# Performance work log

Measured on AMD Instinct MI355X. Metric: run time of the kernel, lower is better.

The kernel has to match this reference:

```python
import jax, jax.numpy as jnp
import numpy as np

N_NODES = 100000
N_EDGES = 1600000
IN_DIM = 128
OUT_DIM = 64


def setup_inputs() -> dict:
    key = jax.random.key(0)
    k1, k2, k3, k4, k5 = jax.random.split(key, 5)
    X = jax.random.normal(k1, (N_NODES, IN_DIM), dtype=jnp.float32)
    # reset_parameters: uniform(-stdv, stdv), stdv = 1/sqrt(output_dim)
    stdv = 1.0 / np.sqrt(OUT_DIM)
    weights = jax.random.uniform(k2, (IN_DIM, OUT_DIM), dtype=jnp.float32,
                                 minval=-stdv, maxval=stdv)
    attention_w = jax.random.normal(k3, (1, 1), dtype=jnp.float32)
    edge_src = jnp.sort(jax.random.randint(k4, (N_EDGES,), 0, N_NODES, dtype=jnp.int32))
    edge_dst = jax.random.randint(k5, (N_EDGES,), 0, N_NODES, dtype=jnp.int32)
    return {"X": X, "weights": weights, "attention_w": attention_w,
            "edge_src": edge_src, "edge_dst": edge_dst}


def reference(X, weights, attention_w, edge_src, edge_dst):
    # Dense projection: X_prime = X @ W  -> [N, OUT_DIM]
    X_prime = X @ weights
    # forward_ef: per-edge scalar feature = <X_prime[src], X_prime[dst]>  -> [E]
    src_feat = X_prime[edge_src]          # [E, OUT_DIM] irregular gather
    dst_feat = X_prime[edge_dst]          # [E, OUT_DIM] irregular gather
    edge_feature = jnp.einsum('ed,ed->e', src_feat, dst_feat)
    # edge_attentions = edge_feature[:, None] @ attention_w -> [n_heads=1, E]
    att = edge_feature * attention_w[0, 0]            # [E]
    # forward_AGNN: out[i] = sum_{e:(i->j)} att[e] * X_prime[j]
    msgs = att[:, None] * dst_feat                    # [E, OUT_DIM]
    out = jax.ops.segment_sum(msgs, edge_src, num_segments=X.shape[0])
    return out
```

## Files before the change

kernel.cpp:

```cpp
#include <hip/hip_runtime.h>
#include <stdint.h>

#define N_NODES 100000
#define N_EDGES 1600000
#define IN_DIM 128
#define OUT_DIM 64

typedef __bf16    bf16x8 __attribute__((ext_vector_type(8)));
typedef float     f32x4  __attribute__((ext_vector_type(4)));
typedef _Float16  h2     __attribute__((ext_vector_type(2)));

__device__ __forceinline__ uint16_t f2bf(float f) {
    uint32_t u = __float_as_uint(f);
    return (uint16_t)((u + 0x7fffu + ((u >> 16) & 1u)) >> 16);
}
__device__ __forceinline__ float hdot8(uint4 a, uint4 b, float c) {
#if __has_builtin(__builtin_amdgcn_fdot2)
    c = __builtin_amdgcn_fdot2(__builtin_bit_cast(h2, a.x), __builtin_bit_cast(h2, b.x), c, false);
    c = __builtin_amdgcn_fdot2(__builtin_bit_cast(h2, a.y), __builtin_bit_cast(h2, b.y), c, false);
    c = __builtin_amdgcn_fdot2(__builtin_bit_cast(h2, a.z), __builtin_bit_cast(h2, b.z), c, false);
    c = __builtin_amdgcn_fdot2(__builtin_bit_cast(h2, a.w), __builtin_bit_cast(h2, b.w), c, false);
#else
    const h2 qa[4] = {__builtin_bit_cast(h2,a.x),__builtin_bit_cast(h2,a.y),
                      __builtin_bit_cast(h2,a.z),__builtin_bit_cast(h2,a.w)};
    const h2 qb[4] = {__builtin_bit_cast(h2,b.x),__builtin_bit_cast(h2,b.y),
                      __builtin_bit_cast(h2,b.z),__builtin_bit_cast(h2,b.w)};
    #pragma unroll
    for (int i = 0; i < 4; ++i) {
        c = fmaf((float)qa[i][0], (float)qb[i][0], c);
        c = fmaf((float)qa[i][1], (float)qb[i][1], c);
    }
#endif
    return c;
}

__global__ __launch_bounds__(256) void prep(const int* __restrict__ src,
                                            const float* __restrict__ W,
                                            int* __restrict__ row_ptr,
                                            uint4* __restrict__ Wfrag) {
    const int b = blockIdx.x;
    if (b < N_EDGES / 256) {
        int e = b * 256 + threadIdx.x;
        int s = src[e];
        if (e == 0) {
            for (int i = 0; i <= s; ++i) row_ptr[i] = 0;
        } else {
            int sp = src[e - 1];
            for (int i = sp + 1; i <= s; ++i) row_ptr[i] = e;
        }
        if (e == N_EDGES - 1) {
            for (int i = s + 1; i <= N_NODES; ++i) row_ptr[i] = N_EDGES;
        }
    } else {
        int item = (b - N_EDGES / 256) * 256 + threadIdx.x;
        if (item < 1024) {
            int f = item >> 6, lane = item & 63;
            int ct = f >> 2, ks = f & 3;
            int col = ct * 16 + (lane & 15);
            int kb  = ks * 32 + (lane >> 4) * 8;
            uint32_t u[4];
            #pragma unroll
            for (int j = 0; j < 4; ++j) {
                uint32_t lo = f2bf(W[(kb + 2 * j)     * OUT_DIM + col]);
                uint32_t hi = f2bf(W[(kb + 2 * j + 1) * OUT_DIM + col]);
                u[j] = lo | (hi << 16);
            }
            Wfrag[f * 64 + lane] = make_uint4(u[0], u[1], u[2], u[3]);
        }
    }
}

__global__ __launch_bounds__(256) void gemm_xw(const float* __restrict__ X,
                                               const uint4* __restrict__ Wfrag,
                                               _Float16* __restrict__ XPh,
                                               int nRows) {
    const int t = threadIdx.x;
    const int lane = t & 63;

    bf16x8 bfr[16];
    #pragma unroll
    for (int f = 0; f < 16; ++f)
        bfr[f] = __builtin_bit_cast(bf16x8, Wfrag[f * 64 + lane]);

    const int rowBase = blockIdx.x * 64 + (t >> 6) * 16;
    const int r  = rowBase + (lane & 15);
    const int kb = (lane >> 4) * 8;
    const bool inb = r < nRows;

    f32x4 acc[4] = {{0,0,0,0},{0,0,0,0},{0,0,0,0},{0,0,0,0}};

    #pragma unroll
    for (int ks = 0; ks < 4; ++ks) {
        float4 x0 = make_float4(0.f,0.f,0.f,0.f), x1 = x0;
        if (inb) {
            const float* p = &X[(size_t)r * IN_DIM + ks * 32 + kb];
            x0 = *(const float4*)&p[0];
            x1 = *(const float4*)&p[4];
        }
        bf16x8 a;
        a[0]=(__bf16)x0.x; a[1]=(__bf16)x0.y; a[2]=(__bf16)x0.z; a[3]=(__bf16)x0.w;
        a[4]=(__bf16)x1.x; a[5]=(__bf16)x1.y; a[6]=(__bf16)x1.z; a[7]=(__bf16)x1.w;
        #pragma unroll
        for (int ct = 0; ct < 4; ++ct)
            acc[ct] = __builtin_amdgcn_mfma_f32_16x16x32_bf16(a, bfr[ct * 4 + ks], acc[ct], 0, 0, 0);
    }

    const int orow = rowBase + (lane >> 4) * 4;
    const int ocol = lane & 15;
    #pragma unroll
    for (int ct = 0; ct < 4; ++ct) {
        #pragma unroll
        for (int rr = 0; rr < 4; ++rr) {
            int gr = orow + rr;
            if (gr < nRows) XPh[(size_t)gr * OUT_DIM + ct * 16 + ocol] = (_Float16)acc[ct][rr];
        }
    }
}

__global__ __launch_bounds__(256, 8) void agnn_edge(const _Float16* __restrict__ XPh,
                                                    const int* __restrict__ row_ptr,
                                                    const int* __restrict__ dst,
                                                    const float* __restrict__ aw,
                                                    float* __restrict__ out) {
    const int t    = threadIdx.x;
    const int lane = t & 63;
    const int g    = lane >> 3;
    const int sl   = lane & 7;
    const int node = blockIdx.x * 32 + (t >> 6) * 8 + g;

    const int lo = row_ptr[node];
    const int hi = row_ptr[node + 1];

    const uint4 q = *(const uint4*)&XPh[(size_t)node * OUT_DIM + sl * 8];
    float acc[8] = {0.f,0.f,0.f,0.f,0.f,0.f,0.f,0.f};

    int  e   = lo;
    bool act = e < hi;
    int  d   = dst[act ? e : 0];
    uint4 xd = *(const uint4*)&XPh[(size_t)d * OUT_DIM + sl * 8];

    while (true) {
        const int  en   = e + 1;
        const bool actn = en < hi;
        const int  dn   = dst[actn ? en : 0];
        const uint4 xdn = *(const uint4*)&XPh[(size_t)dn * OUT_DIM + sl * 8];

        float p = hdot8(q, xd, 0.f);
        p += __shfl_xor(p, 1);
        p += __shfl_xor(p, 2);
        p += __shfl_xor(p, 4);
        p = act ? p : 0.f;
        const h2 d0 = __builtin_bit_cast(h2, xd.x);
        const h2 d1 = __builtin_bit_cast(h2, xd.y);
        const h2 d2 = __builtin_bit_cast(h2, xd.z);
        const h2 d3 = __builtin_bit_cast(h2, xd.w);
        acc[0] = fmaf(p, (float)d0[0], acc[0]);
        acc[1] = fmaf(p, (float)d0[1], acc[1]);
        acc[2] = fmaf(p, (float)d1[0], acc[2]);
        acc[3] = fmaf(p, (float)d1[1], acc[3]);
        acc[4] = fmaf(p, (float)d2[0], acc[4]);
        acc[5] = fmaf(p, (float)d2[1], acc[5]);
        acc[6] = fmaf(p, (float)d3[0], acc[6]);
        acc[7] = fmaf(p, (float)d3[1], acc[7]);

        e = en; act = actn; xd = xdn;
        if (!__any(act)) break;
    }

    const float a = aw[0];
    float* o = &out[(size_t)node * OUT_DIM + sl * 8];
    *(float4*)&o[0] = make_float4(acc[0]*a, acc[1]*a, acc[2]*a, acc[3]*a);
    *(float4*)&o[4] = make_float4(acc[4]*a, acc[5]*a, acc[6]*a, acc[7]*a);
}

extern "C" void kernel_launch(void* const* d_in, const int* in_sizes, int n_in,
                              void* d_out, int out_size, void* d_ws, size_t ws_size,
                              hipStream_t stream) {
    const float* X   = (const float*)d_in[0];
    const float* W   = (const float*)d_in[1];
    const float* aw  = (const float*)d_in[2];
    const int*   src = (const int*)d_in[3];
    const int*   dst = (const int*)d_in[4];
    float* out = (float*)d_out;

    _Float16* XPh     = (_Float16*)d_ws;
    int*      row_ptr = (int*)((char*)d_ws + (size_t)N_NODES * OUT_DIM * 2);
    uint4*    Wfrag   = (uint4*)((char*)d_ws + 13200016);

    prep<<<N_EDGES / 256 + 4, 256, 0, stream>>>(src, W, row_ptr, Wfrag);
    gemm_xw<<<(N_NODES + 63) / 64, 256, 0, stream>>>(X, Wfrag, XPh, N_NODES);
    agnn_edge<<<N_NODES / 32, 256, 0, stream>>>(XPh, row_ptr, dst, aw, out);
}
```

Before: 69.76 us.

## Quantize projected features to int8 and use sdot4 in the edge kernel

The GEMM kernel now also computes a global max-abs of the projected features through an atomicMax. A new kernel quantizes the fp16 features to int8 with one per-tensor scale. A new edge kernel gathers 8-byte int8 rows instead of 16-byte fp16 rows, computes the edge dot products with sdot4, and prefetches two edges ahead; the output is rescaled by scale^3 times the attention weight. This halves the bytes of the irregular gathers, at the cost of an extra quantize pass, an atomic, and much lower numerical precision from per-tensor int8 quantization.

```diff
diff --git a/kernel.cpp b/kernel.cpp
--- a/kernel.cpp
+++ b/kernel.cpp
@@ -13,6 +13,16 @@
 __device__ __forceinline__ uint16_t f2bf(float f) {
     uint32_t u = __float_as_uint(f);
     return (uint16_t)((u + 0x7fffu + ((u >> 16) & 1u)) >> 16);
+}
+__device__ __forceinline__ int dot4i8(uint32_t a, uint32_t b, int c) {
+#if __has_builtin(__builtin_amdgcn_sdot4)
+    return __builtin_amdgcn_sdot4((int)a, (int)b, c, false);
+#else
+    #pragma unroll
+    for (int k = 0; k < 4; ++k)
+        c += (int)(int8_t)(a >> (8 * k)) * (int)(int8_t)(b >> (8 * k));
+    return c;
+#endif
 }
 __device__ __forceinline__ float hdot8(uint4 a, uint4 b, float c) {
 #if __has_builtin(__builtin_amdgcn_fdot2)
@@ -37,7 +47,8 @@
 __global__ __launch_bounds__(256) void prep(const int* __restrict__ src,
                                             const float* __restrict__ W,
                                             int* __restrict__ row_ptr,
-                                            uint4* __restrict__ Wfrag) {
+                                            uint4* __restrict__ Wfrag,
+                                            unsigned* __restrict__ gmax) {
     const int b = blockIdx.x;
     if (b < N_EDGES / 256) {
         int e = b * 256 + threadIdx.x;
@@ -52,6 +63,7 @@
             for (int i = s + 1; i <= N_NODES; ++i) row_ptr[i] = N_EDGES;
         }
     } else {
+        if (b == N_EDGES / 256 && threadIdx.x == 0) *gmax = 0u;
         int item = (b - N_EDGES / 256) * 256 + threadIdx.x;
         if (item < 1024) {
             int f = item >> 6, lane = item & 63;
@@ -73,6 +85,7 @@
 __global__ __launch_bounds__(256) void gemm_xw(const float* __restrict__ X,
                                                const uint4* __restrict__ Wfrag,
                                                _Float16* __restrict__ XPh,
+                                               unsigned* __restrict__ gmax,
                                                int nRows) {
     const int t = threadIdx.x;
     const int lane = t & 63;
@@ -107,14 +120,105 @@
 
     const int orow = rowBase + (lane >> 4) * 4;
     const int ocol = lane & 15;
+    float m = 0.f;
     #pragma unroll
     for (int ct = 0; ct < 4; ++ct) {
         #pragma unroll
         for (int rr = 0; rr < 4; ++rr) {
             int gr = orow + rr;
             if (gr < nRows) XPh[(size_t)gr * OUT_DIM + ct * 16 + ocol] = (_Float16)acc[ct][rr];
-        }
-    }
+            m = fmaxf(m, fabsf(acc[ct][rr]));
+        }
+    }
+    #pragma unroll
+    for (int off = 1; off < 64; off <<= 1) m = fmaxf(m, __shfl_xor(m, off));
+    if (lane == 0) atomicMax(gmax, __float_as_uint(m));
+}
+
+__global__ __launch_bounds__(256) void quantize(const _Float16* __restrict__ XPh,
+                                                const unsigned* __restrict__ gmax,
+                                                uint2* __restrict__ Q) {
+    const int i = blockIdx.x * 256 + threadIdx.x;
+    const float gm = __uint_as_float(*gmax);
+    const float inv = gm > 0.f ? 127.f / gm : 0.f;
+    uint4 h = ((const uint4*)XPh)[i];
+    uint32_t w[2];
+    #pragma unroll
+    for (int half = 0; half < 2; ++half) {
+        uint32_t res = 0;
+        #pragma unroll
+        for (int j = 0; j < 2; ++j) {
+            uint32_t hw = half == 0 ? (j == 0 ? h.x : h.y) : (j == 0 ? h.z : h.w);
+            h2 p = __builtin_bit_cast(h2, hw);
+            int v0 = (int)rintf((float)p[0] * inv);
+            int v1 = (int)rintf((float)p[1] * inv);
+            res |= ((uint32_t)(uint8_t)(int8_t)v0) << (j * 16);
+            res |= ((uint32_t)(uint8_t)(int8_t)v1) << (j * 16 + 8);
+        }
+        w[half] = res;
+    }
+    Q[i] = make_uint2(w[0], w[1]);
+}
+
+__global__ __launch_bounds__(256, 8) void agnn_edge_q(const uint8_t* __restrict__ Q,
+                                                      const int* __restrict__ row_ptr,
+                                                      const int* __restrict__ dst,
+                                                      const float* __restrict__ aw,
+                                                      const unsigned* __restrict__ gmax,
+                                                      float* __restrict__ out) {
+    const int t    = threadIdx.x;
+    const int lane = t & 63;
+    const int g    = lane >> 3;
+    const int sl   = lane & 7;
+    const int node = blockIdx.x * 32 + (t >> 6) * 8 + g;
+
+    const int lo = row_ptr[node];
+    const int hi = row_ptr[node + 1];
+
+    const uint2 q = *(const uint2*)&Q[(size_t)node * OUT_DIM + sl * 8];
+    float acc[8] = {0.f,0.f,0.f,0.f,0.f,0.f,0.f,0.f};
+
+    int  e1 = lo + 1;
+    bool a0 = lo < hi, a1 = e1 < hi;
+    {
+        int d0 = dst[a0 ? lo : 0];
+        int d1 = dst[a1 ? e1 : 0];
+        uint2 x0 = *(const uint2*)&Q[(size_t)d0 * OUT_DIM + sl * 8];
+        uint2 x1 = *(const uint2*)&Q[(size_t)d1 * OUT_DIM + sl * 8];
+
+        while (__any(a0)) {
+            const int  e2 = e1 + 1;
+            const bool a2 = e2 < hi;
+            const int  d2 = dst[a2 ? e2 : 0];
+            const uint2 x2 = *(const uint2*)&Q[(size_t)d2 * OUT_DIM + sl * 8];
+
+            int p = dot4i8(q.x, x0.x, 0);
+            p     = dot4i8(q.y, x0.y, p);
+            p += __shfl_xor(p, 1);
+            p += __shfl_xor(p, 2);
+            p += __shfl_xor(p, 4);
+            const float pf = a0 ? (float)p : 0.f;
+            const int32_t wx = (int32_t)x0.x, wy = (int32_t)x0.y;
+            acc[0] = fmaf(pf, (float)((wx << 24) >> 24), acc[0]);
+            acc[1] = fmaf(pf, (float)((wx << 16) >> 24), acc[1]);
+            acc[2] = fmaf(pf, (float)((wx <<  8) >> 24), acc[2]);
+            acc[3] = fmaf(pf, (float)( wx        >> 24), acc[3]);
+            acc[4] = fmaf(pf, (float)((wy << 24) >> 24), acc[4]);
+            acc[5] = fmaf(pf, (float)((wy << 16) >> 24), acc[5]);
+            acc[6] = fmaf(pf, (float)((wy <<  8) >> 24), acc[6]);
+            acc[7] = fmaf(pf, (float)( wy        >> 24), acc[7]);
+
+            a0 = a1; x0 = x1;
+            a1 = a2; x1 = x2; e1 = e2;
+        }
+    }
+
+    const float gm = __uint_as_float(*gmax);
+    const float s  = gm * (1.f / 127.f);
+    const float k  = s * s * s * aw[0];
+    float* o = &out[(size_t)node * OUT_DIM + sl * 8];
+    *(float4*)&o[0] = make_float4(acc[0]*k, acc[1]*k, acc[2]*k, acc[3]*k);
+    *(float4*)&o[4] = make_float4(acc[4]*k, acc[5]*k, acc[6]*k, acc[7]*k);
 }
 
 __global__ __launch_bounds__(256, 8) void agnn_edge(const _Float16* __restrict__ XPh,
@@ -184,10 +288,18 @@
     float* out = (float*)d_out;
 
     _Float16* XPh     = (_Float16*)d_ws;
-    int*      row_ptr = (int*)((char*)d_ws + (size_t)N_NODES * OUT_DIM * 2);
+    int*      row_ptr = (int*)((char*)d_ws + 12800000);
     uint4*    Wfrag   = (uint4*)((char*)d_ws + 13200016);
-
-    prep<<<N_EDGES / 256 + 4, 256, 0, stream>>>(src, W, row_ptr, Wfrag);
-    gemm_xw<<<(N_NODES + 63) / 64, 256, 0, stream>>>(X, Wfrag, XPh, N_NODES);
-    agnn_edge<<<N_NODES / 32, 256, 0, stream>>>(XPh, row_ptr, dst, aw, out);
-}
+    unsigned* gmax    = (unsigned*)((char*)d_ws + 13216400);
+    uint8_t*  Q       = (uint8_t*)((char*)d_ws + 13216416);
+
+    prep<<<N_EDGES / 256 + 4, 256, 0, stream>>>(src, W, row_ptr, Wfrag, gmax);
+    gemm_xw<<<(N_NODES + 63) / 64, 256, 0, stream>>>(X, Wfrag, XPh, gmax, N_NODES);
+
+    if (ws_size >= (size_t)19616416) {
+        quantize<<<3125, 256, 0, stream>>>(XPh, gmax, (uint2*)Q);
+        agnn_edge_q<<<N_NODES / 32, 256, 0, stream>>>(Q, row_ptr, dst, aw, gmax, out);
+    } else {
+        agnn_edge<<<N_NODES / 32, 256, 0, stream>>>(XPh, row_ptr, dst, aw, out);
+    }
+}
```

Result: slower. 201.8 us (+189.4%).

## Quantize projected features to int8 with per-row scales and batch edge gathers

Applied to the files above, without the earlier changes.

The projection kernel now stores X_prime as int8 with a per-row absmax scale instead of fp16, halving the bytes per gathered row. The edge kernel loads eight destination indices cooperatively, shuffles them across lanes, issues eight independent gathers per step, and computes dot products with sdot4. This targets gather bandwidth and memory-level parallelism in the irregular edge loop, at the cost of int8 quantization error. The dot product is squared into the output, so that error is amplified and may break accuracy tolerance.

```diff
diff --git a/kernel.cpp b/kernel.cpp
--- a/kernel.cpp
+++ b/kernel.cpp
@@ -8,30 +8,20 @@
 
 typedef __bf16    bf16x8 __attribute__((ext_vector_type(8)));
 typedef float     f32x4  __attribute__((ext_vector_type(4)));
-typedef _Float16  h2     __attribute__((ext_vector_type(2)));
 
 __device__ __forceinline__ uint16_t f2bf(float f) {
     uint32_t u = __float_as_uint(f);
     return (uint16_t)((u + 0x7fffu + ((u >> 16) & 1u)) >> 16);
 }
-__device__ __forceinline__ float hdot8(uint4 a, uint4 b, float c) {
-#if __has_builtin(__builtin_amdgcn_fdot2)
-    c = __builtin_amdgcn_fdot2(__builtin_bit_cast(h2, a.x), __builtin_bit_cast(h2, b.x), c, false);
-    c = __builtin_amdgcn_fdot2(__builtin_bit_cast(h2, a.y), __builtin_bit_cast(h2, b.y), c, false);
-    c = __builtin_amdgcn_fdot2(__builtin_bit_cast(h2, a.z), __builtin_bit_cast(h2, b.z), c, false);
-    c = __builtin_amdgcn_fdot2(__builtin_bit_cast(h2, a.w), __builtin_bit_cast(h2, b.w), c, false);
+__device__ __forceinline__ int dot4i8(uint32_t a, uint32_t b, int c) {
+#if __has_builtin(__builtin_amdgcn_sdot4)
+    return __builtin_amdgcn_sdot4((int)a, (int)b, c, false);
 #else
-    const h2 qa[4] = {__builtin_bit_cast(h2,a.x),__builtin_bit_cast(h2,a.y),
-                      __builtin_bit_cast(h2,a.z),__builtin_bit_cast(h2,a.w)};
-    const h2 qb[4] = {__builtin_bit_cast(h2,b.x),__builtin_bit_cast(h2,b.y),
-                      __builtin_bit_cast(h2,b.z),__builtin_bit_cast(h2,b.w)};
-    #pragma unroll
-    for (int i = 0; i < 4; ++i) {
-        c = fmaf((float)qa[i][0], (float)qb[i][0], c);
-        c = fmaf((float)qa[i][1], (float)qb[i][1], c);
-    }
+    #pragma unroll
+    for (int k = 0; k < 4; ++k)
+        c += (int)(int8_t)(a >> (8 * k)) * (int)(int8_t)(b >> (8 * k));
+    return c;
 #endif
-    return c;
 }
 
 __global__ __launch_bounds__(256) void prep(const int* __restrict__ src,
@@ -70,10 +60,11 @@
     }
 }
 
-__global__ __launch_bounds__(256) void gemm_xw(const float* __restrict__ X,
-                                               const uint4* __restrict__ Wfrag,
-                                               _Float16* __restrict__ XPh,
-                                               int nRows) {
+__global__ __launch_bounds__(256) void gemm_q(const float* __restrict__ X,
+                                              const uint4* __restrict__ Wfrag,
+                                              uint8_t* __restrict__ Q,
+                                              float* __restrict__ scales,
+                                              int nRows) {
     const int t = threadIdx.x;
     const int lane = t & 63;
 
@@ -108,20 +99,33 @@
     const int orow = rowBase + (lane >> 4) * 4;
     const int ocol = lane & 15;
     #pragma unroll
-    for (int ct = 0; ct < 4; ++ct) {
-        #pragma unroll
-        for (int rr = 0; rr < 4; ++rr) {
-            int gr = orow + rr;
-            if (gr < nRows) XPh[(size_t)gr * OUT_DIM + ct * 16 + ocol] = (_Float16)acc[ct][rr];
-        }
-    }
-}
-
-__global__ __launch_bounds__(256, 8) void agnn_edge(const _Float16* __restrict__ XPh,
-                                                    const int* __restrict__ row_ptr,
-                                                    const int* __restrict__ dst,
-                                                    const float* __restrict__ aw,
-                                                    float* __restrict__ out) {
+    for (int rr = 0; rr < 4; ++rr) {
+        float m = fmaxf(fmaxf(fabsf(acc[0][rr]), fabsf(acc[1][rr])),
+                        fmaxf(fabsf(acc[2][rr]), fabsf(acc[3][rr])));
+        m = fmaxf(m, __shfl_xor(m, 1));
+        m = fmaxf(m, __shfl_xor(m, 2));
+        m = fmaxf(m, __shfl_xor(m, 4));
+        m = fmaxf(m, __shfl_xor(m, 8));
+        const float inv = m > 0.f ? 127.f / m : 0.f;
+        const int gr = orow + rr;
+        if (gr < nRows) {
+            if (ocol == 0) scales[gr] = m * (1.f / 127.f);
+            #pragma unroll
+            for (int ct = 0; ct < 4; ++ct) {
+                int v = (int)rintf(acc[ct][rr] * inv);
+                v = min(127, max(-127, v));
+                Q[(size_t)gr * OUT_DIM + ct * 16 + ocol] = (uint8_t)(int8_t)v;
+            }
+        }
+    }
+}
+
+__global__ __launch_bounds__(256, 8) void agnn_edge_q(const uint8_t* __restrict__ Q,
+                                                      const float* __restrict__ scales,
+                                                      const int* __restrict__ row_ptr,
+                                                      const int* __restrict__ dst,
+                                                      const float* __restrict__ aw,
+                                                      float* __restrict__ out) {
     const int t    = threadIdx.x;
     const int lane = t & 63;
     const int g    = lane >> 3;
@@ -131,46 +135,53 @@
     const int lo = row_ptr[node];
     const int hi = row_ptr[node + 1];
 
-    const uint4 q = *(const uint4*)&XPh[(size_t)node * OUT_DIM + sl * 8];
+    const uint2 q = *(const uint2*)&Q[(size_t)node * OUT_DIM + sl * 8];
     float acc[8] = {0.f,0.f,0.f,0.f,0.f,0.f,0.f,0.f};
 
-    int  e   = lo;
-    bool act = e < hi;
-    int  d   = dst[act ? e : 0];
-    uint4 xd = *(const uint4*)&XPh[(size_t)d * OUT_DIM + sl * 8];
-
-    while (true) {
-        const int  en   = e + 1;
-        const bool actn = en < hi;
-        const int  dn   = dst[actn ? en : 0];
-        const uint4 xdn = *(const uint4*)&XPh[(size_t)dn * OUT_DIM + sl * 8];
-
-        float p = hdot8(q, xd, 0.f);
-        p += __shfl_xor(p, 1);
-        p += __shfl_xor(p, 2);
-        p += __shfl_xor(p, 4);
-        p = act ? p : 0.f;
-        const h2 d0 = __builtin_bit_cast(h2, xd.x);
-        const h2 d1 = __builtin_bit_cast(h2, xd.y);
-        const h2 d2 = __builtin_bit_cast(h2, xd.z);
-        const h2 d3 = __builtin_bit_cast(h2, xd.w);
-        acc[0] = fmaf(p, (float)d0[0], acc[0]);
-        acc[1] = fmaf(p, (float)d0[1], acc[1]);
-        acc[2] = fmaf(p, (float)d1[0], acc[2]);
-        acc[3] = fmaf(p, (float)d1[1], acc[3]);
-        acc[4] = fmaf(p, (float)d2[0], acc[4]);
-        acc[5] = fmaf(p, (float)d2[1], acc[5]);
-        acc[6] = fmaf(p, (float)d3[0], acc[6]);
-        acc[7] = fmaf(p, (float)d3[1], acc[7]);
-
-        e = en; act = actn; xd = xdn;
-        if (!__any(act)) break;
-    }
-
-    const float a = aw[0];
+    int base = lo;
+    while (__any(base < hi)) {
+        const int nj = hi - base;
+        int myd = 0;
+        if (base < hi) myd = dst[min(base + sl, hi - 1)];
+
+        uint2 x[8];
+        float s2[8];
+        #pragma unroll
+        for (int j = 0; j < 8; ++j) {
+            x[j]  = make_uint2(0u, 0u);
+            s2[j] = 0.f;
+            if (j < nj) {
+                const int dj = __shfl(myd, g * 8 + j);
+                x[j] = *(const uint2*)&Q[(size_t)dj * OUT_DIM + sl * 8];
+                const float sj = scales[dj];
+                s2[j] = sj * sj;
+            }
+        }
+        #pragma unroll
+        for (int j = 0; j < 8; ++j) {
+            int p = dot4i8(q.x, x[j].x, 0);
+            p     = dot4i8(q.y, x[j].y, p);
+            p += __shfl_xor(p, 1);
+            p += __shfl_xor(p, 2);
+            p += __shfl_xor(p, 4);
+            const float f = (float)p * s2[j];
+            const int32_t wx = (int32_t)x[j].x, wy = (int32_t)x[j].y;
+            acc[0] = fmaf(f, (float)((wx << 24) >> 24), acc[0]);
+            acc[1] = fmaf(f, (float)((wx << 16) >> 24), acc[1]);
+            acc[2] = fmaf(f, (float)((wx <<  8) >> 24), acc[2]);
+            acc[3] = fmaf(f, (float)( wx        >> 24), acc[3]);
+            acc[4] = fmaf(f, (float)((wy << 24) >> 24), acc[4]);
+            acc[5] = fmaf(f, (float)((wy << 16) >> 24), acc[5]);
+            acc[6] = fmaf(f, (float)((wy <<  8) >> 24), acc[6]);
+            acc[7] = fmaf(f, (float)( wy        >> 24), acc[7]);
+        }
+        base += 8;
+    }
+
+    const float k = scales[node] * aw[0];
     float* o = &out[(size_t)node * OUT_DIM + sl * 8];
-    *(float4*)&o[0] = make_float4(acc[0]*a, acc[1]*a, acc[2]*a, acc[3]*a);
-    *(float4*)&o[4] = make_float4(acc[4]*a, acc[5]*a, acc[6]*a, acc[7]*a);
+    *(float4*)&o[0] = make_float4(acc[0]*k, acc[1]*k, acc[2]*k, acc[3]*k);
+    *(float4*)&o[4] = make_float4(acc[4]*k, acc[5]*k, acc[6]*k, acc[7]*k);
 }
 
 extern "C" void kernel_launch(void* const* d_in, const int* in_sizes, int n_in,
@@ -183,11 +194,12 @@
     const int*   dst = (const int*)d_in[4];
     float* out = (float*)d_out;
 
-    _Float16* XPh     = (_Float16*)d_ws;
-    int*      row_ptr = (int*)((char*)d_ws + (size_t)N_NODES * OUT_DIM * 2);
-    uint4*    Wfrag   = (uint4*)((char*)d_ws + 13200016);
+    uint8_t* Q       = (uint8_t*)d_ws;
+    float*   scales  = (float*)((char*)d_ws + 6400000);
+    int*     row_ptr = (int*)((char*)d_ws + 6800000);
+    uint4*   Wfrag   = (uint4*)((char*)d_ws + 7200016);
 
     prep<<<N_EDGES / 256 + 4, 256, 0, stream>>>(src, W, row_ptr, Wfrag);
-    gemm_xw<<<(N_NODES + 63) / 64, 256, 0, stream>>>(X, Wfrag, XPh, N_NODES);
-    agnn_edge<<<N_NODES / 32, 256, 0, stream>>>(XPh, row_ptr, dst, aw, out);
-}
+    gemm_q<<<(N_NODES + 63) / 64, 256, 0, stream>>>(X, Wfrag, Q, scales, N_NODES);
+    agnn_edge_q<<<N_NODES / 32, 256, 0, stream>>>(Q, scales, row_ptr, dst, aw, out);
+}
```

Result: faster. 63.81 us (-8.5%).
